# Optimization experiments

Hardware: AMD Instinct MI355X
Metric: run time of the kernel (lower is better)

## Reference

```python
import jax, jax.numpy as jnp
import numpy as np

V, N, D, K = 4, 2048, 128, 10
NEG = -1e9


def setup_inputs() -> dict:
    key = jax.random.key(0)
    k1, k2, k3, k4, k5 = jax.random.split(key, 5)
    aligned = jax.random.normal(k1, (V, N, D), dtype=jnp.float32)
    C = jax.random.uniform(k2, (V, V, N, N), dtype=jnp.float32)
    s = 1.0 / np.sqrt(D)
    WQ = jax.random.normal(k3, (V, D, D), dtype=jnp.float32) * s
    WK = jax.random.normal(k4, (V, D, D), dtype=jnp.float32) * s
    WV = jax.random.normal(k5, (V, D, D), dtype=jnp.float32) * s
    return {"aligned": aligned, "C": C, "WQ": WQ, "WK": WK, "WV": WV}


def _forward(aligned, C, WQ, WK, WV):
    # per-view linear projections (nn.Linear: x @ W^T), W: (V, out, in)
    Qn = jnp.einsum('vnd,ved->vne', aligned, WQ)  # (V,N,D)
    Kn = jnp.einsum('vnd,ved->vne', aligned, WK)
    Vn = jnp.einsum('vnd,ved->vne', aligned, WV)

    # per-pair row-wise top-k sparsify + row-normalize
    vals, idx = jax.lax.top_k(C, K)  # (V,V,N,K)
    pi = jnp.arange(V)[:, None, None, None]
    qi = jnp.arange(V)[None, :, None, None]
    ri = jnp.arange(N)[None, None, :, None]
    sparse = jnp.zeros_like(C).at[pi, qi, ri, idx].set(vals)
    row_sum = sparse.sum(axis=3, keepdims=True) + 1e-12
    C_hat = sparse / row_sum
    # diagonal (p == q) blocks stay all-zero in the original loop
    offdiag = (1.0 - jnp.eye(V, dtype=C.dtype))[:, :, None, None]
    C_hat = C_hat * offdiag

    # full pairwise scores (p queries attend to q keys)
    scores = jnp.einsum('pnd,qmd->pqnm', Qn, Kn) / jnp.sqrt(jnp.float32(D))
    mask = (C_hat > 0).astype(scores.dtype)
    scores = scores * mask + (1.0 - mask) * NEG
    alpha = jax.nn.softmax(scores, axis=3)  # (V,V,N,N)

    # aggregate: sum over source views q (diagonal gives uniform avg of Vn[p])
    nbr = jnp.einsum('pqnm,qmd->pnd', alpha, Vn)  # (V,N,D)
    return nbr


def reference(aligned, C, WQ, WK, WV):
    return _forward(aligned, C, WQ, WK, WV)
```

## Files before the change

kernel.cpp:

```cpp
#include <hip/hip_runtime.h>
#include <cstdint>
#include <cstddef>

#define VV 4
#define NN 2048
#define DDIM 128
#define KK 10
#define CAP 256

#define WAVE_LDS_SYNC() asm volatile("s_waitcnt lgkmcnt(0)" ::: "memory")

__device__ __forceinline__ bool kgt(float v1, int i1, float v0, int i0) {
  return (v1 > v0) || (v1 == v0 && i1 < i0);
}

__global__ __launch_bounds__(256) void proj_kernel(
    const float* __restrict__ A, const float* __restrict__ WQ,
    const float* __restrict__ WK, const float* __restrict__ WV,
    float* __restrict__ Qn, float* __restrict__ Kn, float* __restrict__ Vn,
    float* __restrict__ partialMV)
{
  __shared__ float As[16][DDIM];
  __shared__ float Ws[3][16][129];
  __shared__ float s_mv[2][DDIM];

  const int t    = threadIdx.x;
  const int v    = blockIdx.x >> 7;
  const int blk  = blockIdx.x & 127;
  const int n0   = blk * 16;
  const int e    = t & 127;
  const int half = t >> 7;

  float accq[8], acck[8], accv[8];
#pragma unroll
  for (int r = 0; r < 8; ++r) { accq[r] = 0.f; acck[r] = 0.f; accv[r] = 0.f; }

  const float* Ab = A + ((size_t)v * NN + n0) * DDIM;
#pragma unroll
  for (int k = 0; k < 2; ++k) {
    int id4 = k * 256 + t;
    int r   = id4 >> 5;
    int d4  = id4 & 31;
    float4 a4 = *(const float4*)(Ab + (size_t)id4 * 4);
    *(float4*)&As[r][d4 * 4] = a4;
  }
  const float* wqb = WQ + (size_t)v * DDIM * DDIM;
  const float* wkb = WK + (size_t)v * DDIM * DDIM;
  const float* wvb = WV + (size_t)v * DDIM * DDIM;

  for (int d0 = 0; d0 < DDIM; d0 += 16) {
    __syncthreads();
#pragma unroll
    for (int k = 0; k < 2; ++k) {
      int id4 = k * 256 + t;
      int ee  = id4 >> 2;
      int c4  = id4 & 3;
      const float4 wq4 = *(const float4*)(wqb + (size_t)ee * DDIM + d0 + c4 * 4);
      const float4 wk4 = *(const float4*)(wkb + (size_t)ee * DDIM + d0 + c4 * 4);
      const float4 wv4 = *(const float4*)(wvb + (size_t)ee * DDIM + d0 + c4 * 4);
      int dd = c4 * 4;
      Ws[0][dd + 0][ee] = wq4.x; Ws[0][dd + 1][ee] = wq4.y;
      Ws[0][dd + 2][ee] = wq4.z; Ws[0][dd + 3][ee] = wq4.w;
      Ws[1][dd + 0][ee] = wk4.x; Ws[1][dd + 1][ee] = wk4.y;
      Ws[1][dd + 2][ee] = wk4.z; Ws[1][dd + 3][ee] = wk4.w;
      Ws[2][dd + 0][ee] = wv4.x; Ws[2][dd + 1][ee] = wv4.y;
      Ws[2][dd + 2][ee] = wv4.z; Ws[2][dd + 3][ee] = wv4.w;
    }
    __syncthreads();
#pragma unroll
    for (int dd = 0; dd < 16; dd += 4) {
      float4 a[8];
#pragma unroll
      for (int r = 0; r < 8; ++r) a[r] = *(const float4*)&As[half * 8 + r][d0 + dd];
#pragma unroll
      for (int c = 0; c < 4; ++c) {
        float wq = Ws[0][dd + c][e];
        float wk = Ws[1][dd + c][e];
        float wv = Ws[2][dd + c][e];
#pragma unroll
        for (int r = 0; r < 8; ++r) {
          float av = ((const float*)&a[r])[c];
          accq[r] = fmaf(av, wq, accq[r]);
          acck[r] = fmaf(av, wk, acck[r]);
          accv[r] = fmaf(av, wv, accv[r]);
        }
      }
    }
  }

  const size_t ob = ((size_t)v * NN + n0 + half * 8) * DDIM + e;
#pragma unroll
  for (int r = 0; r < 8; ++r) {
    Qn[ob + (size_t)r * DDIM] = accq[r];
    Kn[ob + (size_t)r * DDIM] = acck[r];
    Vn[ob + (size_t)r * DDIM] = accv[r];
  }
  float s = 0.f;
#pragma unroll
  for (int r = 0; r < 8; ++r) s += accv[r];
  s_mv[half][e] = s;
  __syncthreads();
  if (half == 0)
    partialMV[((size_t)v * 128 + blk) * DDIM + e] = s + s_mv[1][e];
}

__global__ __launch_bounds__(128) void meanv_kernel(
    const float* __restrict__ partialMV, float* __restrict__ meanV)
{
  const int v = blockIdx.x;
  const int e = threadIdx.x;
  const float* pb = partialMV + (size_t)v * 128 * DDIM + e;
  float s0 = 0.f, s1 = 0.f, s2 = 0.f, s3 = 0.f;
#pragma unroll 8
  for (int b = 0; b < 128; b += 4) {
    s0 += pb[(size_t)(b + 0) * DDIM];
    s1 += pb[(size_t)(b + 1) * DDIM];
    s2 += pb[(size_t)(b + 2) * DDIM];
    s3 += pb[(size_t)(b + 3) * DDIM];
  }
  meanV[v * DDIM + e] = (s0 + s1 + s2 + s3) * (1.0f / 2048.0f);
}

__global__ __launch_bounds__(256) void fused_kernel(
    const float* __restrict__ C, const float* __restrict__ Qn,
    const float* __restrict__ Kn, const float* __restrict__ Vn,
    const float* __restrict__ meanV, float* __restrict__ out)
{
  __shared__ float    s_val[4][CAP];
  __shared__ int      s_idx[4][CAP];
  __shared__ unsigned s_cnt[4];
  __shared__ float    s_sc[4][32];
  __shared__ float    s_al[4][32];
  __shared__ int      s_sel[4][32];
  __shared__ __align__(16) float s_mv[DDIM];

  const int t    = threadIdx.x;
  const int w    = t >> 6;
  const int lane = t & 63;
  const int task = blockIdx.x * 4 + w;
  const int p    = task >> 11;
  const int n    = task & 2047;
  const float SCALE = 0.08838834764831845f;

  if (t < DDIM) s_mv[t] = meanV[p * DDIM + t];
  __syncthreads();

  for (int o = 0; o < 3; ++o) {
    const int q = o + (o >= p ? 1 : 0);
    const float* row = C + (((size_t)(p * 4 + q) * NN + n) << 11);
    float4 vv[8];
#pragma unroll
    for (int i = 0; i < 8; ++i) vv[i] = *(const float4*)(row + i * 256 + lane * 4);
    if (lane == 0) s_cnt[w] = 0u;

    const float T1 = 0.99f, T2 = 0.95f;
    int c1 = 0;
#pragma unroll
    for (int i = 0; i < 8; ++i) {
      const float* pv = (const float*)&vv[i];
#pragma unroll
      for (int c = 0; c < 4; ++c) c1 += (pv[c] > T1) ? 1 : 0;
    }
#pragma unroll
    for (int off = 32; off; off >>= 1) c1 += __shfl_xor(c1, off);

    float T = T1; int cnt = c1; bool ok = (c1 >= KK && c1 <= CAP);
    if (!ok) {
      int c2 = 0;
#pragma unroll
      for (int i = 0; i < 8; ++i) {
        const float* pv = (const float*)&vv[i];
#pragma unroll
        for (int c = 0; c < 4; ++c) c2 += (pv[c] > T2) ? 1 : 0;
      }
#pragma unroll
      for (int off = 32; off; off >>= 1) c2 += __shfl_xor(c2, off);
      T = T2; cnt = c2; ok = (c2 >= KK && c2 <= CAP);
    }

    if (ok) {
#pragma unroll
      for (int i = 0; i < 8; ++i) {
        const float* pv = (const float*)&vv[i];
#pragma unroll
        for (int c = 0; c < 4; ++c) {
          float x = pv[c];
          if (x > T) {
            unsigned pos = atomicAdd(&s_cnt[w], 1u);
            s_val[w][pos] = x;
            s_idx[w][pos] = i * 256 + lane * 4 + c;
          }
        }
      }
      WAVE_LDS_SYNC();
      if (cnt <= 64) {
        float kv = (lane < cnt) ? s_val[w][lane] : -1e30f;
        int   ki = (lane < cnt) ? s_idx[w][lane] : 0x7FFFFFFF;
#pragma unroll
        for (int k = 2; k <= 64; k <<= 1) {
#pragma unroll
          for (int j = k >> 1; j > 0; j >>= 1) {
            float ov = __shfl_xor(kv, j);
            int   oi = __shfl_xor(ki, j);
            bool dirDesc = (lane & k) == 0;
            bool lower   = (lane & j) == 0;
            bool ogt     = (ov > kv) || (ov == kv && oi < ki);
            bool take    = (dirDesc == lower) ? ogt : !ogt;
            if (take) { kv = ov; ki = oi; }
          }
        }
        if (lane < KK) s_sel[w][o * KK + lane] = ki;
      } else {
        float rv[4]; int ri[4];
#pragma unroll
        for (int s = 0; s < 4; ++s) {
          int  sl = lane + s * 64;
          bool in = sl < cnt;
          rv[s] = in ? s_val[w][sl] : -1e30f;
          ri[s] = in ? s_idx[w][sl] : 0x7FFFFFFF;
        }
        for (int r = 0; r < KK; ++r) {
          float lv = rv[0]; int li = ri[0]; int ls = 0;
#pragma unroll
          for (int s = 1; s < 4; ++s)
            if (kgt(rv[s], ri[s], lv, li)) { lv = rv[s]; li = ri[s]; ls = s; }
          float mv = lv; int mi = li;
#pragma unroll
          for (int off = 1; off < 64; off <<= 1) {
            float ov = __shfl_xor(mv, off);
            int   oi = __shfl_xor(mi, off);
            if (kgt(ov, oi, mv, mi)) { mv = ov; mi = oi; }
          }
          if (lane == 0) s_sel[w][o * KK + r] = mi;
          if (li == mi) {
#pragma unroll
            for (int s = 0; s < 4; ++s)
              if (ls == s) { rv[s] = -1e30f; ri[s] = 0x7FFFFFFF; }
          }
        }
      }
    } else {
      unsigned consumed = 0;
      for (int r = 0; r < KK; ++r) {
        float lv = -1e30f; int li = 0x7FFFFFFF; int ls = 0;
#pragma unroll
        for (int i = 0; i < 8; ++i) {
          const float* pv = (const float*)&vv[i];
#pragma unroll
          for (int c = 0; c < 4; ++c) {
            int   sl = i * 4 + c;
            float x  = ((consumed >> sl) & 1u) ? -1e30f : pv[c];
            int   ix = i * 256 + lane * 4 + c;
            if (kgt(x, ix, lv, li)) { lv = x; li = ix; ls = sl; }
          }
        }
        float mv = lv; int mi = li;
#pragma unroll
        for (int off = 1; off < 64; off <<= 1) {
          float ov = __shfl_xor(mv, off);
          int   oi = __shfl_xor(mi, off);
          if (kgt(ov, oi, mv, mi)) { mv = ov; mi = oi; }
        }
        if (lane == 0) s_sel[w][o * KK + r] = mi;
        if (li == mi) consumed |= (1u << ls);
      }
    }
    WAVE_LDS_SYNC();
  }

  const float* qrow = Qn + ((size_t)p * NN + n) * DDIM;
  float2 q2 = *(const float2*)(qrow + 2 * lane);
  q2.x *= SCALE; q2.y *= SCALE;

#pragma unroll
  for (int o = 0; o < 3; ++o) {
    const int q = o + (o >= p ? 1 : 0);
    const float* Kb = Kn + (size_t)q * NN * DDIM;
    int    sel[KK];
    float2 kv2[KK];
#pragma unroll
    for (int j = 0; j < KK; ++j) {
      sel[j] = s_sel[w][o * KK + j];
      kv2[j] = *(const float2*)(Kb + (size_t)sel[j] * DDIM + 2 * lane);
    }
#pragma unroll
    for (int j = 0; j < KK; ++j) {
      float s = q2.x * kv2[j].x + q2.y * kv2[j].y;
#pragma unroll
      for (int off = 32; off; off >>= 1) s += __shfl_xor(s, off);
      if (lane == 0) s_sc[w][o * KK + j] = s;
    }
  }
  WAVE_LDS_SYNC();

  if (lane < 30) {
    const int b = (lane / KK) * KK;
    float m = s_sc[w][b];
#pragma unroll
    for (int j = 1; j < KK; ++j) m = fmaxf(m, s_sc[w][b + j]);
    float den = 0.f;
#pragma unroll
    for (int j = 0; j < KK; ++j) den += __expf(s_sc[w][b + j] - m);
    s_al[w][lane] = __expf(s_sc[w][lane] - m) / den;
  }
  WAVE_LDS_SYNC();

  float2 acc = *(const float2*)&s_mv[2 * lane];
#pragma unroll
  for (int o = 0; o < 3; ++o) {
    const int q = o + (o >= p ? 1 : 0);
    const float* Vb = Vn + (size_t)q * NN * DDIM;
    float2 vv2[KK]; float al[KK];
#pragma unroll
    for (int j = 0; j < KK; ++j) {
      int s  = s_sel[w][o * KK + j];
      al[j]  = s_al[w][o * KK + j];
      vv2[j] = *(const float2*)(Vb + (size_t)s * DDIM + 2 * lane);
    }
#pragma unroll
    for (int j = 0; j < KK; ++j) {
      acc.x = fmaf(al[j], vv2[j].x, acc.x);
      acc.y = fmaf(al[j], vv2[j].y, acc.y);
    }
  }
  float* orow = out + ((size_t)p * NN + n) * DDIM;
  *(float2*)(orow + 2 * lane) = acc;
}

extern "C" void kernel_launch(void* const* d_in, const int* in_sizes, int n_in,
                              void* d_out, int out_size, void* d_ws, size_t ws_size,
                              hipStream_t stream)
{
  const float* A  = (const float*)d_in[0];
  const float* C  = (const float*)d_in[1];
  const float* WQ = (const float*)d_in[2];
  const float* WK = (const float*)d_in[3];
  const float* WV = (const float*)d_in[4];
  float* out = (float*)d_out;

  char* ws = (char*)d_ws;
  float* Qn        = (float*)ws;
  float* Kn        = (float*)(ws + (size_t)4 * 1024 * 1024);
  float* Vn        = (float*)(ws + (size_t)8 * 1024 * 1024);
  float* partialMV = (float*)(ws + (size_t)12 * 1024 * 1024);
  float* meanV     = (float*)(ws + (size_t)12 * 1024 * 1024 + 256 * 1024);

  hipLaunchKernelGGL(proj_kernel, dim3(512), dim3(256), 0, stream,
                     A, WQ, WK, WV, Qn, Kn, Vn, partialMV);
  hipLaunchKernelGGL(meanv_kernel, dim3(4), dim3(128), 0, stream,
                     partialMV, meanV);
  hipLaunchKernelGGL(fused_kernel, dim3(2048), dim3(256), 0, stream,
                     C, Qn, Kn, Vn, meanV, out);
}
```

Baseline: 396.2 us.

## Prefetch next C row into LDS via async global_load_lds during top-k

Loads the first C row into registers and issues async global-to-LDS loads for the next source view's row, so the top-k selection of one row overlaps with fetching the next. Q and meanV are loaded up front into registers, which removes the shared s_mv buffer and the block-wide barrier. This adds 32 KB of LDS per block, which may reduce occupancy, and it relies on manual vmcnt/lgkmcnt waits for correctness.

```diff
diff --git a/kernel.cpp b/kernel.cpp
--- a/kernel.cpp
+++ b/kernel.cpp
@@ -9,6 +9,11 @@
 #define CAP 256
 
 #define WAVE_LDS_SYNC() asm volatile("s_waitcnt lgkmcnt(0)" ::: "memory")
+
+#define GLOAD_LDS(gptr, lptr)                                      \
+  __builtin_amdgcn_global_load_lds(                                \
+      (const __attribute__((address_space(1))) void*)(gptr),       \
+      (__attribute__((address_space(3))) void*)(lptr), 16, 0, 0)
 
 __device__ __forceinline__ bool kgt(float v1, int i1, float v0, int i0) {
   return (v1 > v0) || (v1 == v0 && i1 < i0);
@@ -126,13 +131,13 @@
     const float* __restrict__ Kn, const float* __restrict__ Vn,
     const float* __restrict__ meanV, float* __restrict__ out)
 {
+  __shared__ float    s_buf[4][2048];
   __shared__ float    s_val[4][CAP];
   __shared__ int      s_idx[4][CAP];
   __shared__ unsigned s_cnt[4];
   __shared__ float    s_sc[4][32];
   __shared__ float    s_al[4][32];
   __shared__ int      s_sel[4][32];
-  __shared__ __align__(16) float s_mv[DDIM];
 
   const int t    = threadIdx.x;
   const int w    = t >> 6;
@@ -142,15 +147,25 @@
   const int n    = task & 2047;
   const float SCALE = 0.08838834764831845f;
 
-  if (t < DDIM) s_mv[t] = meanV[p * DDIM + t];
-  __syncthreads();
+  const int q_0 = (0 >= p) ? 1 : 0;
+  const int q_1 = (1 >= p) ? 2 : 1;
+  const int q_2 = (2 >= p) ? 3 : 2;
+  const float* row0 = C + (((size_t)(p * 4 + q_0) * NN + n) << 11);
+  const float* row1 = C + (((size_t)(p * 4 + q_1) * NN + n) << 11);
+  const float* row2 = C + (((size_t)(p * 4 + q_2) * NN + n) << 11);
+  float* buf = s_buf[w];
+
+  float4 vv[8];
+#pragma unroll
+  for (int i = 0; i < 8; ++i) vv[i] = *(const float4*)(row0 + i * 256 + lane * 4);
+#pragma unroll
+  for (int i = 0; i < 8; ++i) GLOAD_LDS(row1 + i * 256 + lane * 4, buf + i * 256);
+  const float* qrow = Qn + ((size_t)p * NN + n) * DDIM;
+  float2 q2 = *(const float2*)(qrow + 2 * lane);
+  float2 mv2 = *(const float2*)(meanV + p * DDIM + 2 * lane);
+  q2.x *= SCALE; q2.y *= SCALE;
 
   for (int o = 0; o < 3; ++o) {
-    const int q = o + (o >= p ? 1 : 0);
-    const float* row = C + (((size_t)(p * 4 + q) * NN + n) << 11);
-    float4 vv[8];
-#pragma unroll
-    for (int i = 0; i < 8; ++i) vv[i] = *(const float4*)(row + i * 256 + lane * 4);
     if (lane == 0) s_cnt[w] = 0u;
 
     const float T1 = 0.99f, T2 = 0.95f;
@@ -266,11 +281,19 @@
       }
     }
     WAVE_LDS_SYNC();
-  }
-
-  const float* qrow = Qn + ((size_t)p * NN + n) * DDIM;
-  float2 q2 = *(const float2*)(qrow + 2 * lane);
-  q2.x *= SCALE; q2.y *= SCALE;
+
+    if (o < 2) {
+      asm volatile("s_waitcnt vmcnt(0)" ::: "memory");
+#pragma unroll
+      for (int i = 0; i < 8; ++i) vv[i] = *(const float4*)&buf[i * 256 + lane * 4];
+      asm volatile("s_waitcnt lgkmcnt(0)" ::: "memory");
+      if (o == 0) {
+#pragma unroll
+        for (int i = 0; i < 8; ++i)
+          GLOAD_LDS(row2 + i * 256 + lane * 4, buf + i * 256);
+      }
+    }
+  }
 
 #pragma unroll
   for (int o = 0; o < 3; ++o) {
@@ -305,7 +328,7 @@
   }
   WAVE_LDS_SYNC();
 
-  float2 acc = *(const float2*)&s_mv[2 * lane];
+  float2 acc = mv2;
 #pragma unroll
   for (int o = 0; o < 3; ++o) {
     const int q = o + (o >= p ? 1 : 0);
```

Result: slower. 405.7 us (+2.4%).

## Stream C rows without register buffering and drop block-wide meanV staging

Applied to the files above, without the earlier changes.

The fused kernel no longer holds the whole 2048-float C row in 32 registers per lane. Each pass now streams the row from global memory and does the threshold count and the compaction into LDS in a single pass with a CAP guard. It also raises launch bounds to 6 waves per EU, loads meanV and Q directly into registers instead of staging meanV in LDS behind a __syncthreads, and fuses one multiply into an fma. The aim is lower register pressure and higher occupancy. The cost is re-reading C whenever the fallback threshold or the full-scan path runs, and extra atomic traffic when the count overflows.

```diff
diff --git a/kernel.cpp b/kernel.cpp
--- a/kernel.cpp
+++ b/kernel.cpp
@@ -121,7 +121,7 @@
   meanV[v * DDIM + e] = (s0 + s1 + s2 + s3) * (1.0f / 2048.0f);
 }
 
-__global__ __launch_bounds__(256) void fused_kernel(
+__global__ __launch_bounds__(256, 6) void fused_kernel(
     const float* __restrict__ C, const float* __restrict__ Qn,
     const float* __restrict__ Kn, const float* __restrict__ Vn,
     const float* __restrict__ meanV, float* __restrict__ out)
@@ -132,7 +132,6 @@
   __shared__ float    s_sc[4][32];
   __shared__ float    s_al[4][32];
   __shared__ int      s_sel[4][32];
-  __shared__ __align__(16) float s_mv[DDIM];
 
   const int t    = threadIdx.x;
   const int w    = t >> 6;
@@ -142,57 +141,63 @@
   const int n    = task & 2047;
   const float SCALE = 0.08838834764831845f;
 
-  if (t < DDIM) s_mv[t] = meanV[p * DDIM + t];
-  __syncthreads();
+  const float* qrow = Qn + ((size_t)p * NN + n) * DDIM;
+  float2 q2 = *(const float2*)(qrow + 2 * lane);
+  float2 mv2 = *(const float2*)(meanV + p * DDIM + 2 * lane);
+  q2.x *= SCALE; q2.y *= SCALE;
 
   for (int o = 0; o < 3; ++o) {
     const int q = o + (o >= p ? 1 : 0);
     const float* row = C + (((size_t)(p * 4 + q) * NN + n) << 11);
-    float4 vv[8];
-#pragma unroll
-    for (int i = 0; i < 8; ++i) vv[i] = *(const float4*)(row + i * 256 + lane * 4);
-    if (lane == 0) s_cnt[w] = 0u;
 
     const float T1 = 0.99f, T2 = 0.95f;
-    int c1 = 0;
-#pragma unroll
-    for (int i = 0; i < 8; ++i) {
-      const float* pv = (const float*)&vv[i];
-#pragma unroll
-      for (int c = 0; c < 4; ++c) c1 += (pv[c] > T1) ? 1 : 0;
-    }
-#pragma unroll
-    for (int off = 32; off; off >>= 1) c1 += __shfl_xor(c1, off);
-
-    float T = T1; int cnt = c1; bool ok = (c1 >= KK && c1 <= CAP);
+    int cnt;
+    {
+      if (lane == 0) s_cnt[w] = 0u;
+      WAVE_LDS_SYNC();
+#pragma unroll
+      for (int i = 0; i < 8; ++i) {
+        float4 vv = *(const float4*)(row + i * 256 + lane * 4);
+        const float* pv = (const float*)&vv;
+#pragma unroll
+        for (int c = 0; c < 4; ++c) {
+          if (pv[c] > T1) {
+            unsigned pos = atomicAdd(&s_cnt[w], 1u);
+            if (pos < CAP) {
+              s_val[w][pos] = pv[c];
+              s_idx[w][pos] = i * 256 + lane * 4 + c;
+            }
+          }
+        }
+      }
+      WAVE_LDS_SYNC();
+      cnt = (int)s_cnt[w];
+    }
+    bool ok = (cnt >= KK && cnt <= CAP);
     if (!ok) {
-      int c2 = 0;
+      if (lane == 0) s_cnt[w] = 0u;
+      WAVE_LDS_SYNC();
 #pragma unroll
       for (int i = 0; i < 8; ++i) {
-        const float* pv = (const float*)&vv[i];
-#pragma unroll
-        for (int c = 0; c < 4; ++c) c2 += (pv[c] > T2) ? 1 : 0;
-      }
-#pragma unroll
-      for (int off = 32; off; off >>= 1) c2 += __shfl_xor(c2, off);
-      T = T2; cnt = c2; ok = (c2 >= KK && c2 <= CAP);
+        float4 vv = *(const float4*)(row + i * 256 + lane * 4);
+        const float* pv = (const float*)&vv;
+#pragma unroll
+        for (int c = 0; c < 4; ++c) {
+          if (pv[c] > T2) {
+            unsigned pos = atomicAdd(&s_cnt[w], 1u);
+            if (pos < CAP) {
+              s_val[w][pos] = pv[c];
+              s_idx[w][pos] = i * 256 + lane * 4 + c;
+            }
+          }
+        }
+      }
+      WAVE_LDS_SYNC();
+      cnt = (int)s_cnt[w];
+      ok  = (cnt >= KK && cnt <= CAP);
     }
 
     if (ok) {
-#pragma unroll
-      for (int i = 0; i < 8; ++i) {
-        const float* pv = (const float*)&vv[i];
-#pragma unroll
-        for (int c = 0; c < 4; ++c) {
-          float x = pv[c];
-          if (x > T) {
-            unsigned pos = atomicAdd(&s_cnt[w], 1u);
-            s_val[w][pos] = x;
-            s_idx[w][pos] = i * 256 + lane * 4 + c;
-          }
-        }
-      }
-      WAVE_LDS_SYNC();
       if (cnt <= 64) {
         float kv = (lane < cnt) ? s_val[w][lane] : -1e30f;
         int   ki = (lane < cnt) ? s_idx[w][lane] : 0x7FFFFFFF;
@@ -245,7 +250,8 @@
         float lv = -1e30f; int li = 0x7FFFFFFF; int ls = 0;
 #pragma unroll
         for (int i = 0; i < 8; ++i) {
-          const float* pv = (const float*)&vv[i];
+          float4 vv = *(const float4*)(row + i * 256 + lane * 4);
+          const float* pv = (const float*)&vv;
 #pragma unroll
           for (int c = 0; c < 4; ++c) {
             int   sl = i * 4 + c;
@@ -268,10 +274,6 @@
     WAVE_LDS_SYNC();
   }
 
-  const float* qrow = Qn + ((size_t)p * NN + n) * DDIM;
-  float2 q2 = *(const float2*)(qrow + 2 * lane);
-  q2.x *= SCALE; q2.y *= SCALE;
-
 #pragma unroll
   for (int o = 0; o < 3; ++o) {
     const int q = o + (o >= p ? 1 : 0);
@@ -285,7 +287,7 @@
     }
 #pragma unroll
     for (int j = 0; j < KK; ++j) {
-      float s = q2.x * kv2[j].x + q2.y * kv2[j].y;
+      float s = fmaf(q2.x, kv2[j].x, q2.y * kv2[j].y);
 #pragma unroll
       for (int off = 32; off; off >>= 1) s += __shfl_xor(s, off);
       if (lane == 0) s_sc[w][o * KK + j] = s;
@@ -305,7 +307,7 @@
   }
   WAVE_LDS_SYNC();
 
-  float2 acc = *(const float2*)&s_mv[2 * lane];
+  float2 acc = mv2;
 #pragma unroll
   for (int o = 0; o < 3; ++o) {
     const int q = o + (o >= p ? 1 : 0);
```

New measurement: 472.5 us. 1.19x slower.
